# Kernel tuning notes

Hardware: AMD Instinct MI355X
Metric: run time of the kernel (lower is better)

The kernel has to match this reference:

```python
import jax, jax.numpy as jnp
import numpy as np

B, T, C, H, W_SP = 16, 256, 1024, 8, 8
OUT = 1024
ALPHA_INIT = 0.9


def setup_inputs() -> dict:
    key = jax.random.key(0)
    k_x, k_w = jax.random.split(key, 2)
    x = jax.random.normal(k_x, (B, T, C, H, W_SP), dtype=jnp.float32)
    r0 = jnp.zeros((B, OUT), dtype=jnp.float32)
    W = jax.random.normal(k_w, (OUT, C), dtype=jnp.float32) * 0.02
    b = jnp.zeros((OUT,), dtype=jnp.float32)
    alpha = jnp.full((OUT,), ALPHA_INIT, dtype=jnp.float32)
    return {"x": x, "r0": r0, "W": W, "b": b, "alpha": alpha}


def reference(x, r0, W, b, alpha):
    # x: [B, T, C, H, W] -> spatial mean -> [B, T, C]
    xm = x.mean(axis=(3, 4))
    # per-timestep linear done as one batched matmul: [B, T, OUT]
    u = jnp.einsum('btc,oc->bto', xm, W) + b
    # linear diagonal recurrence r_t = alpha * r_{t-1} + u_t
    def step(r, u_t):
        r = alpha * r + u_t
        return r, r
    r_final, r_seq = jax.lax.scan(step, r0, jnp.swapaxes(u, 0, 1))  # scan over T
    r_seq = jnp.swapaxes(r_seq, 0, 1)  # [B, T, OUT]
    return (r_seq, r_final)
```

## Files before the change

kernel.cpp:

```cpp
#include <hip/hip_runtime.h>
#include <hip/hip_bf16.h>
#include <stdint.h>


typedef __attribute__((ext_vector_type(8))) short bf16x8;
typedef __attribute__((ext_vector_type(4))) float f32x4;

__device__ __forceinline__ unsigned short f2bf(float f) {
  union { float f; unsigned int u; } c; c.f = f;
  unsigned int u = c.u;
  return (unsigned short)((u + 0x7FFFu + ((u >> 16) & 1u)) >> 16);
}

__global__ __launch_bounds__(256) void k_mean(const float* __restrict__ x,
                                              unsigned short* __restrict__ xm,
                                              const float* __restrict__ W,
                                              unsigned short* __restrict__ Wb) {
  const int tid = threadIdx.x;
  const int wi = blockIdx.x * 256 + tid;
  if (wi < 262144) {
    float4 v = *(const float4*)(W + wi * 4);
    ushort4 o;
    o.x = f2bf(v.x); o.y = f2bf(v.y); o.z = f2bf(v.z); o.w = f2bf(v.w);
    *(ushort4*)(Wb + wi * 4) = o;
  }
  const int sub = tid & 15;
  const int grp = tid >> 4;
  for (int base = blockIdx.x * 16; base < (1 << 22); base += gridDim.x * 16) {
    int seg = base + grp;
    const float4 v = *(const float4*)(x + (long)seg * 64 + sub * 4);
    float s = v.x + v.y + v.z + v.w;
    s += __shfl_xor(s, 1);
    s += __shfl_xor(s, 2);
    s += __shfl_xor(s, 4);
    s += __shfl_xor(s, 8);
    if (sub == 0) xm[seg] = f2bf(s * 0.015625f);
  }
}

#define GLDS16(g, l) \
  __builtin_amdgcn_global_load_lds((const __attribute__((address_space(1))) void*)(g), \
                                   (__attribute__((address_space(3))) void*)(l), 16, 0, 0)

__global__ __launch_bounds__(256, 1) void k_gemmscan(const unsigned short* __restrict__ A,
                                                     const unsigned short* __restrict__ Bm,
                                                     const float* __restrict__ bias,
                                                     const float* __restrict__ r0,
                                                     const float* __restrict__ alpha,
                                                     float* __restrict__ out) {
  __shared__ unsigned short lds[2][20480];
  const int bid = blockIdx.x;
  const int nb  = (bid & 7) * 32 + (bid >> 3);
  const int b   = nb >> 4;
  const int n0  = (nb & 15) * 64;
  const int m0  = b * 256;

  const int tid  = threadIdx.x;
  const int lane = tid & 63;
  const int w    = tid >> 6;
  const int r16  = lane & 15;
  const int kb   = lane >> 4;
  const int h    = lane >> 4;

  f32x4 acc[4][4] = {};

  const int srow8  = tid >> 3;
  const int sslot8 = tid & 7;
  const int gkoff  = (sslot8 ^ (srow8 & 7)) << 3;

  const unsigned short* ag[8];
  const unsigned short* bg[2];
#pragma unroll
  for (int ra = 0; ra < 8; ra++) ag[ra] = A  + (long)(m0 + ra * 32 + srow8) * 1024 + gkoff;
#pragma unroll
  for (int rb = 0; rb < 2; rb++) bg[rb] = Bm + (long)(n0 + rb * 32 + srow8) * 1024 + gkoff;

  auto stage = [&](int t) {
    const int k0 = t * 64;
    char* Ab = (char*)&lds[t & 1][0];
    char* Bb = (char*)&lds[t & 1][16384];
#pragma unroll
    for (int ra = 0; ra < 8; ra++) GLDS16(ag[ra] + k0, Ab + tid * 16 + ra * 4096);
#pragma unroll
    for (int rb = 0; rb < 2; rb++) GLDS16(bg[rb] + k0, Bb + tid * 16 + rb * 4096);
  };

  auto compute = [&](int t) {
    const unsigned short* Ab = &lds[t & 1][0];
    const unsigned short* Bb = &lds[t & 1][16384];
    bf16x8 af[2][4], bf_[2][4];
#pragma unroll
    for (int ks = 0; ks < 2; ks++) {
#pragma unroll
      for (int i = 0; i < 4; i++) {
        const int rr = w * 64 + i * 16 + r16;
        af[ks][i] = *(const bf16x8*)(Ab + rr * 64 + (((ks * 4 + kb) ^ (rr & 7)) << 3));
      }
#pragma unroll
      for (int j = 0; j < 4; j++) {
        const int cc = j * 16 + r16;
        bf_[ks][j] = *(const bf16x8*)(Bb + cc * 64 + (((ks * 4 + kb) ^ (cc & 7)) << 3));
      }
    }
#pragma unroll
    for (int ks = 0; ks < 2; ks++)
#pragma unroll
      for (int i = 0; i < 4; i++)
#pragma unroll
        for (int j = 0; j < 4; j++)
          acc[i][j] = __builtin_amdgcn_mfma_f32_16x16x32_bf16(af[ks][i], bf_[ks][j], acc[i][j], 0, 0, 0);
  };

  stage(0);
  __syncthreads();
#pragma unroll 1
  for (int t = 0; t < 16; t++) {
    if (t < 15) stage(t + 1);
    compute(t);
    __syncthreads();
  }

  float a1[4], a2[4], a3[4], a4[4], a8[4], a12[4], a16[4], a64[4], p4h[4], r0v[4], Cw[4];
#pragma unroll
  for (int j = 0; j < 4; j++) {
    const int col = n0 + j * 16 + r16;
    const float a = alpha[col];
    a1[j] = a; a2[j] = a * a; a3[j] = a2[j] * a; a4[j] = a2[j] * a2[j];
    a8[j] = a4[j] * a4[j]; a12[j] = a8[j] * a4[j]; a16[j] = a8[j] * a8[j];
    const float a32 = a16[j] * a16[j]; a64[j] = a32 * a32;
    p4h[j] = (h == 0) ? 1.f : (h == 1) ? a4[j] : (h == 2) ? a8[j] : a12[j];
    r0v[j] = r0[b * 1024 + col];
    const float bb = bias[col];
    Cw[j] = 0.f;
#pragma unroll
    for (int i = 0; i < 4; i++) {
      const float u0 = acc[i][j][0] + bb, u1 = acc[i][j][1] + bb;
      const float u2 = acc[i][j][2] + bb, u3 = acc[i][j][3] + bb;
      const float l0 = u0;
      const float l1 = fmaf(a1[j], l0, u1);
      const float l2 = fmaf(a1[j], l1, u2);
      const float l3 = fmaf(a1[j], l2, u3);
      float xv = l3;
      float t1 = __shfl_up(xv, 16); if (h >= 1) xv = fmaf(a4[j], t1, xv);
      float t2 = __shfl_up(xv, 32); if (h >= 2) xv = fmaf(a8[j], t2, xv);
      float P  = __shfl_up(xv, 16); if (h == 0) P = 0.f;
      const float G = fmaf(p4h[j], Cw[j], P);
      acc[i][j][0] = fmaf(a1[j], G, l0);
      acc[i][j][1] = fmaf(a2[j], G, l1);
      acc[i][j][2] = fmaf(a3[j], G, l2);
      acc[i][j][3] = fmaf(a4[j], G, l3);
      const float xe = __shfl(xv, r16 + 48);
      Cw[j] = fmaf(a16[j], Cw[j], xe);
    }
  }

  float* F = (float*)&lds[0][0];
  if (h == 0) {
#pragma unroll
    for (int j = 0; j < 4; j++) F[w * 64 + j * 16 + r16] = Cw[j];
  }
  __syncthreads();
  float R[4];
#pragma unroll
  for (int j = 0; j < 4; j++) {
    R[j] = r0v[j];
    for (int v = 0; v < w; v++) R[j] = fmaf(a64[j], R[j], F[v * 64 + j * 16 + r16]);
    float gi = p4h[j] * R[j];
#pragma unroll
    for (int i = 0; i < 4; i++) {
      acc[i][j][0] = fmaf(a1[j], gi, acc[i][j][0]);
      acc[i][j][1] = fmaf(a2[j], gi, acc[i][j][1]);
      acc[i][j][2] = fmaf(a3[j], gi, acc[i][j][2]);
      acc[i][j][3] = fmaf(a4[j], gi, acc[i][j][3]);
      gi *= a16[j];
    }
  }

#pragma unroll
  for (int i = 0; i < 4; i++)
#pragma unroll
    for (int j = 0; j < 4; j++) {
      const long mrow = m0 + w * 64 + i * 16 + h * 4;
      const int  n    = n0 + j * 16 + r16;
#pragma unroll
      for (int q = 0; q < 4; q++)
        out[(mrow + q) * 1024 + n] = acc[i][j][q];
    }
  if (w == 3 && h == 0) {
#pragma unroll
    for (int j = 0; j < 4; j++)
      out[(1 << 22) + b * 1024 + n0 + j * 16 + r16] = fmaf(a64[j], R[j], F[192 + j * 16 + r16]);
  }
}

extern "C" void kernel_launch(void* const* d_in, const int* in_sizes, int n_in,
                              void* d_out, int out_size, void* d_ws, size_t ws_size,
                              hipStream_t stream) {
  const float* x     = (const float*)d_in[0];
  const float* r0    = (const float*)d_in[1];
  const float* W     = (const float*)d_in[2];
  const float* b     = (const float*)d_in[3];
  const float* alpha = (const float*)d_in[4];
  float* out = (float*)d_out;

  unsigned short* xm = (unsigned short*)d_ws;
  unsigned short* Wb = (unsigned short*)((char*)d_ws + (8u << 20));

  k_mean<<<2048, 256, 0, stream>>>(x, xm, W, Wb);
  k_gemmscan<<<256, 256, 0, stream>>>(xm, Wb, b, r0, alpha, out);
}
```

Baseline: 228.3 us.

## Load GEMM fragments directly from global memory instead of LDS staging

Removes the double-buffered global_load_lds staging and its per-step barriers. Each wave now reads its A and B MFMA fragments straight from global memory (through L1/L2), and the LDS footprint shrinks to a small scratch for the scan carry. This drops the LDS round trip and barrier overhead. The cost is that B fragments shared by all four waves are fetched redundantly, loads are less coalesced, and no explicit prefetch overlaps memory with compute.

```diff
diff --git a/kernel.cpp b/kernel.cpp
--- a/kernel.cpp
+++ b/kernel.cpp
@@ -38,69 +38,43 @@
   }
 }
 
-#define GLDS16(g, l) \
-  __builtin_amdgcn_global_load_lds((const __attribute__((address_space(1))) void*)(g), \
-                                   (__attribute__((address_space(3))) void*)(l), 16, 0, 0)
-
-__global__ __launch_bounds__(256, 1) void k_gemmscan(const unsigned short* __restrict__ A,
-                                                     const unsigned short* __restrict__ Bm,
-                                                     const float* __restrict__ bias,
-                                                     const float* __restrict__ r0,
-                                                     const float* __restrict__ alpha,
-                                                     float* __restrict__ out) {
-  __shared__ unsigned short lds[2][20480];
+__global__ __launch_bounds__(256) void k_gemmscan(const unsigned short* __restrict__ A,
+                                                  const unsigned short* __restrict__ Bm,
+                                                  const float* __restrict__ bias,
+                                                  const float* __restrict__ r0,
+                                                  const float* __restrict__ alpha,
+                                                  float* __restrict__ out) {
+  __shared__ float F[256];
   const int bid = blockIdx.x;
   const int nb  = (bid & 7) * 32 + (bid >> 3);
   const int b   = nb >> 4;
   const int n0  = (nb & 15) * 64;
   const int m0  = b * 256;
 
-  const int tid  = threadIdx.x;
-  const int lane = tid & 63;
-  const int w    = tid >> 6;
+  const int lane = threadIdx.x & 63;
+  const int w    = threadIdx.x >> 6;
   const int r16  = lane & 15;
   const int kb   = lane >> 4;
-  const int h    = lane >> 4;
+  const int h    = kb;
 
   f32x4 acc[4][4] = {};
 
-  const int srow8  = tid >> 3;
-  const int sslot8 = tid & 7;
-  const int gkoff  = (sslot8 ^ (srow8 & 7)) << 3;
+  const unsigned short* ap[4];
+  const unsigned short* bp[4];
+#pragma unroll
+  for (int i = 0; i < 4; i++) ap[i] = A  + (long)(m0 + w * 64 + i * 16 + r16) * 1024 + kb * 8;
+#pragma unroll
+  for (int j = 0; j < 4; j++) bp[j] = Bm + (long)(n0 + j * 16 + r16) * 1024 + kb * 8;
 
-  const unsigned short* ag[8];
-  const unsigned short* bg[2];
-#pragma unroll
-  for (int ra = 0; ra < 8; ra++) ag[ra] = A  + (long)(m0 + ra * 32 + srow8) * 1024 + gkoff;
-#pragma unroll
-  for (int rb = 0; rb < 2; rb++) bg[rb] = Bm + (long)(n0 + rb * 32 + srow8) * 1024 + gkoff;
-
-  auto stage = [&](int t) {
-    const int k0 = t * 64;
-    char* Ab = (char*)&lds[t & 1][0];
-    char* Bb = (char*)&lds[t & 1][16384];
-#pragma unroll
-    for (int ra = 0; ra < 8; ra++) GLDS16(ag[ra] + k0, Ab + tid * 16 + ra * 4096);
-#pragma unroll
-    for (int rb = 0; rb < 2; rb++) GLDS16(bg[rb] + k0, Bb + tid * 16 + rb * 4096);
-  };
-
-  auto compute = [&](int t) {
-    const unsigned short* Ab = &lds[t & 1][0];
-    const unsigned short* Bb = &lds[t & 1][16384];
+#pragma unroll 2
+  for (int t = 0; t < 16; t++) {
     bf16x8 af[2][4], bf_[2][4];
 #pragma unroll
     for (int ks = 0; ks < 2; ks++) {
 #pragma unroll
-      for (int i = 0; i < 4; i++) {
-        const int rr = w * 64 + i * 16 + r16;
-        af[ks][i] = *(const bf16x8*)(Ab + rr * 64 + (((ks * 4 + kb) ^ (rr & 7)) << 3));
-      }
+      for (int i = 0; i < 4; i++) af[ks][i] = *(const bf16x8*)(ap[i] + t * 64 + ks * 32);
 #pragma unroll
-      for (int j = 0; j < 4; j++) {
-        const int cc = j * 16 + r16;
-        bf_[ks][j] = *(const bf16x8*)(Bb + cc * 64 + (((ks * 4 + kb) ^ (cc & 7)) << 3));
-      }
+      for (int j = 0; j < 4; j++) bf_[ks][j] = *(const bf16x8*)(bp[j] + t * 64 + ks * 32);
     }
 #pragma unroll
     for (int ks = 0; ks < 2; ks++)
@@ -109,15 +83,6 @@
 #pragma unroll
         for (int j = 0; j < 4; j++)
           acc[i][j] = __builtin_amdgcn_mfma_f32_16x16x32_bf16(af[ks][i], bf_[ks][j], acc[i][j], 0, 0, 0);
-  };
-
-  stage(0);
-  __syncthreads();
-#pragma unroll 1
-  for (int t = 0; t < 16; t++) {
-    if (t < 15) stage(t + 1);
-    compute(t);
-    __syncthreads();
   }
 
   float a1[4], a2[4], a3[4], a4[4], a8[4], a12[4], a16[4], a64[4], p4h[4], r0v[4], Cw[4];
@@ -154,7 +119,6 @@
     }
   }
 
-  float* F = (float*)&lds[0][0];
   if (h == 0) {
 #pragma unroll
     for (int j = 0; j < 4; j++) F[w * 64 + j * 16 + r16] = Cw[j];
```

Measured after the change: 247.3 us. 8.3% more time.
